# Kernel tuning notes

Measured on AMD Instinct MI355X. Metric: run time of the kernel, lower is better.

The kernel has to match this reference:

```python
import jax, jax.numpy as jnp
import numpy as np

C = 64        # number of classes (rows of mu)
K = 64        # int(d * overlap_ratio) = int(128 * 0.5)
ALPHA = 1.0   # margin


def _pairdist(mu, x):
    # Euclidean distance from every center to every sample: [C, N]
    d2 = (mu * mu).sum(-1)[:, None] + (x * x).sum(-1)[None, :] - 2.0 * (mu @ x.T)
    return jnp.sqrt(jnp.maximum(d2, 0.0))


def setup_inputs() -> dict:
    key = jax.random.key(0)
    k1, k2, k3 = jax.random.split(key, 3)
    N, D = 131072, 256
    x = jax.random.normal(k1, (N, D), dtype=jnp.float32)
    y = jax.random.randint(k2, (N, 3), 0, C)
    # ensure every class 0..C-1 is present with ~equal counts (matches torch.unique)
    y = y.at[:, 2].set(jnp.arange(N) % C)
    mu = jax.random.normal(k3, (C, D), dtype=jnp.float32)
    return {"x": x, "y": y, "mu": mu}


def reference(x, y, mu):
    labels = y[:, 2]                                     # [N]
    D = _pairdist(mu, x)                                 # [C, N]
    mask = labels[None, :] == jnp.arange(C)[:, None]     # [C, N] class membership

    # pos: per class c, K LARGEST distances from center c to its own samples
    pos_vals = jax.lax.top_k(jnp.where(mask, D, -jnp.inf), K)[0]  # [C, K]
    pos_mean = pos_vals.mean(-1)                                  # [C]

    # neg: for each sample-class c2, K SMALLEST distances from every center c1
    def neg_for_class(m):  # m: [N] bool mask for class c2
        vals = jax.lax.top_k(jnp.where(m[None, :], -D, -jnp.inf), K)[0]  # [C, K]
        return (-vals).mean(-1)  # [C] smallest-K mean per center c1

    negM = jax.lax.map(neg_for_class, mask)              # [C2, C1]

    hinge = jnp.maximum(ALPHA + pos_mean[None, :] - negM, 0.0)  # [C2, C1]
    offdiag = 1.0 - jnp.eye(C, dtype=hinge.dtype)
    loss = (hinge * offdiag).sum() / x.shape[0]
    return loss
```

## Files before the change

kernel.cpp:

```cpp
#include <hip/hip_runtime.h>
#include <math.h>


#define DDIM 256
#define CC 64
#define KSEL 64
#define TPTS 128
#define XS 40
#define SELN 2048

typedef short s4v __attribute__((ext_vector_type(4)));
typedef short s8v __attribute__((ext_vector_type(8)));
typedef float f4v __attribute__((ext_vector_type(4)));

__device__ __forceinline__ void cvt_split(float f, short& h, short& l) {
  const unsigned int u = __float_as_uint(f);
  const unsigned int hb = (u + 0x7FFFu + ((u >> 16) & 1u)) >> 16;
  h = (short)hb;
  const float rem = f - __uint_as_float(hb << 16);
  const unsigned int ur = __float_as_uint(rem);
  l = (short)((ur + 0x7FFFu + ((ur >> 16) & 1u)) >> 16);
}

__global__ __launch_bounds__(256) void prepK(const float* __restrict__ mu, short* __restrict__ mhG,
                                             short* __restrict__ mlG, float* __restrict__ mn2G,
                                             int* __restrict__ cnts) {
  const int b = blockIdx.x, t = threadIdx.x;
  if (b == 0 && t < 128) cnts[t] = 0;
  const int row = b * 4 + (t >> 6), l = t & 63;
  const float4 v = *reinterpret_cast<const float4*>(mu + (size_t)row * DDIM + l * 4);
  const float vs[4] = {v.x, v.y, v.z, v.w};
  s4v hv, lv;
  float s2 = 0.f;
  #pragma unroll
  for (int j = 0; j < 4; ++j) {
    short hj, lj; cvt_split(vs[j], hj, lj);
    hv[j] = hj; lv[j] = lj;
    s2 = fmaf(vs[j], vs[j], s2);
  }
  *reinterpret_cast<s4v*>(&mhG[(size_t)row * DDIM + l * 4]) = hv;
  *reinterpret_cast<s4v*>(&mlG[(size_t)row * DDIM + l * 4]) = lv;
  #pragma unroll
  for (int off = 32; off > 0; off >>= 1) s2 += __shfl_xor(s2, off, 64);
  if (l == 0) mn2G[row] = s2;
}

__global__ __launch_bounds__(256) void countK(const int* __restrict__ y, int* cnt, int N) {
  int i = blockIdx.x * 256 + threadIdx.x;
  if (i < N) atomicAdd(&cnt[y[3 * i + 2] & (CC - 1)], 1);
}

__global__ void scanK(const int* __restrict__ cnt, int* base) {
  if (threadIdx.x == 0) {
    int s = 0;
    for (int i = 0; i < CC; ++i) { base[i] = s; s += cnt[i]; }
  }
}

__global__ __launch_bounds__(256) void fillK(const int* __restrict__ y, const int* __restrict__ base,
                                             int* cnt2, int* idxs, int N) {
  int i = blockIdx.x * 256 + threadIdx.x;
  if (i < N) {
    int m = y[3 * i + 2] & (CC - 1);
    int r = atomicAdd(&cnt2[m], 1);
    idxs[base[m] + r] = i;
  }
}

__global__ __launch_bounds__(256, 4) void distK(const float* __restrict__ x, const short* __restrict__ mhG,
                                                const short* __restrict__ mlG, const float* __restrict__ mn2G,
                                                const int* __restrict__ idxs, float* __restrict__ Dg, int N) {
  __shared__ __align__(16) short xh[TPTS][XS];
  __shared__ __align__(16) short xl[TPTS][XS];
  __shared__ int pid[TPTS];
  __shared__ float xn2[TPTS];

  const int t = threadIdx.x;
  const int wgp0 = blockIdx.x * TPTS;
  if (t < TPTS) pid[t] = idxs[wgp0 + t];

  const int q = t & 7, pr = t >> 3;
  const int w = t >> 6, l = t & 63;
  const int lr = l & 15, lk = l >> 4;

  f4v acc[4][2];
  #pragma unroll
  for (int a = 0; a < 4; ++a)
    #pragma unroll
    for (int b = 0; b < 2; ++b) acc[a][b] = (f4v)0.f;
  float xnacc[4] = {0.f, 0.f, 0.f, 0.f};

  __syncthreads();
  int pidr[4];
  #pragma unroll
  for (int p = 0; p < 4; ++p) pidr[p] = pid[p * 32 + pr];

  float4 vreg[4];
  #pragma unroll
  for (int p = 0; p < 4; ++p)
    vreg[p] = *reinterpret_cast<const float4*>(x + (size_t)pidr[p] * DDIM + q * 4);

  for (int ch = 0; ch < 8; ++ch) {
    const int kb = ch * 32;
    s8v ah[4], al_[4];
    #pragma unroll
    for (int mt = 0; mt < 4; ++mt) {
      const size_t ro = (size_t)(mt * 16 + lr) * DDIM + kb + lk * 8;
      ah[mt]  = *reinterpret_cast<const s8v*>(mhG + ro);
      al_[mt] = *reinterpret_cast<const s8v*>(mlG + ro);
    }
    #pragma unroll
    for (int p = 0; p < 4; ++p) {
      const float vs[4] = {vreg[p].x, vreg[p].y, vreg[p].z, vreg[p].w};
      s4v hv, lv;
      float s2 = 0.f;
      #pragma unroll
      for (int j = 0; j < 4; ++j) {
        short hj, lj; cvt_split(vs[j], hj, lj);
        hv[j] = hj; lv[j] = lj;
        s2 = fmaf(vs[j], vs[j], s2);
      }
      xnacc[p] += s2;
      const int pt = p * 32 + pr;
      *reinterpret_cast<s4v*>(&xh[pt][q * 4]) = hv;
      *reinterpret_cast<s4v*>(&xl[pt][q * 4]) = lv;
    }
    __syncthreads();
    if (ch < 7) {
      #pragma unroll
      for (int p = 0; p < 4; ++p)
        vreg[p] = *reinterpret_cast<const float4*>(x + (size_t)pidr[p] * DDIM + kb + 32 + q * 4);
    }
    s8v bh[2], bl[2];
    #pragma unroll
    for (int nt = 0; nt < 2; ++nt) {
      const int prow = w * 32 + nt * 16 + lr;
      bh[nt] = *reinterpret_cast<const s8v*>(&xh[prow][lk * 8]);
      bl[nt] = *reinterpret_cast<const s8v*>(&xl[prow][lk * 8]);
    }
    #pragma unroll
    for (int mt = 0; mt < 4; ++mt) {
      #pragma unroll
      for (int nt = 0; nt < 2; ++nt) {
        acc[mt][nt] = __builtin_amdgcn_mfma_f32_16x16x32_bf16(ah[mt],  bh[nt], acc[mt][nt], 0, 0, 0);
        acc[mt][nt] = __builtin_amdgcn_mfma_f32_16x16x32_bf16(ah[mt],  bl[nt], acc[mt][nt], 0, 0, 0);
        acc[mt][nt] = __builtin_amdgcn_mfma_f32_16x16x32_bf16(al_[mt], bh[nt], acc[mt][nt], 0, 0, 0);
      }
    }
    __syncthreads();
  }
  #pragma unroll
  for (int p = 0; p < 4; ++p) {
    float s = xnacc[p];
    s += __shfl_xor(s, 1, 64); s += __shfl_xor(s, 2, 64); s += __shfl_xor(s, 4, 64);
    if (q == 0) xn2[p * 32 + pr] = s;
  }
  __syncthreads();
  #pragma unroll
  for (int mt = 0; mt < 4; ++mt) {
    #pragma unroll
    for (int r = 0; r < 4; ++r) {
      const int m = mt * 16 + lk * 4 + r;
      const float mn = mn2G[m];
      #pragma unroll
      for (int nt = 0; nt < 2; ++nt) {
        const int p = w * 32 + nt * 16 + lr;
        const float d2 = mn + xn2[p] - 2.f * acc[mt][nt][r];
        Dg[(size_t)m * N + wgp0 + p] = sqrtf(fmaxf(d2, 0.f));
      }
    }
  }
}

__global__ __launch_bounds__(128) void selK(const float* __restrict__ Dg, const int* __restrict__ cnt,
                                            const int* __restrict__ base, float* __restrict__ posM,
                                            float* __restrict__ neg, int N) {
  __shared__ __align__(16) unsigned int keys[SELN];
  __shared__ unsigned int sh_lo, sh_hi;
  __shared__ int sh_cnt[2];
  __shared__ float sh_sum[2];
  const int c = blockIdx.x, m = blockIdx.y;
  const int t = threadIdx.x;
  const int w = t >> 6, lane = t & 63;
  const bool diag = (c == m);
  int cm = cnt[m]; if (cm > SELN) cm = SELN;
  const int bm = base[m];
  const float* src = Dg + (size_t)c * N + bm;
  const int cm4 = (cm + 3) & ~3;

  unsigned int kmin = 0xFFFFFFFFu, kmax = 0u;
  for (int i = t; i < cm4; i += 128) {
    unsigned int key = 0xFFFFFFFFu;
    if (i < cm) {
      const unsigned int b = __float_as_uint(src[i]);
      key = diag ? ~b : b;
      kmin = min(kmin, key); kmax = max(kmax, key);
    }
    keys[i] = key;
  }
  #pragma unroll
  for (int off = 32; off > 0; off >>= 1) {
    kmin = min(kmin, (unsigned int)__shfl_xor((int)kmin, off, 64));
    kmax = max(kmax, (unsigned int)__shfl_xor((int)kmax, off, 64));
  }
  if (lane == 0) { sh_cnt[w] = (int)kmin; sh_sum[w] = __uint_as_float(kmax); }
  __syncthreads();
  if (t == 0) {
    sh_lo = min((unsigned int)sh_cnt[0], (unsigned int)sh_cnt[1]);
    sh_hi = max(__float_as_uint(sh_sum[0]), __float_as_uint(sh_sum[1]));
  }

  for (;;) {
    __syncthreads();
    const unsigned int lo = sh_lo, hi = sh_hi;
    if (lo >= hi) break;
    const unsigned int mid = lo + ((hi - lo) >> 1);
    int cl = 0;
    for (int i4 = t * 4; i4 < cm4; i4 += 512) {
      const uint4 kv = *reinterpret_cast<const uint4*>(&keys[i4]);
      cl += (int)(kv.x <= mid) + (int)(kv.y <= mid) + (int)(kv.z <= mid) + (int)(kv.w <= mid);
    }
    #pragma unroll
    for (int off = 32; off > 0; off >>= 1) cl += __shfl_xor(cl, off, 64);
    if (lane == 0) sh_cnt[w] = cl;
    __syncthreads();
    if (t == 0) {
      if (sh_cnt[0] + sh_cnt[1] >= KSEL) sh_hi = mid; else sh_lo = mid + 1;
    }
  }
  const unsigned int kth = sh_lo;

  int cl = 0; float sl = 0.f;
  for (int i4 = t * 4; i4 < cm4; i4 += 512) {
    const uint4 kv = *reinterpret_cast<const uint4*>(&keys[i4]);
    const unsigned int ks[4] = {kv.x, kv.y, kv.z, kv.w};
    #pragma unroll
    for (int j = 0; j < 4; ++j) {
      if (ks[j] < kth) { ++cl; sl += __uint_as_float(diag ? ~ks[j] : ks[j]); }
    }
  }
  #pragma unroll
  for (int off = 32; off > 0; off >>= 1) {
    cl += __shfl_xor(cl, off, 64);
    sl += __shfl_xor(sl, off, 64);
  }
  if (lane == 0) { sh_cnt[w] = cl; sh_sum[w] = sl; }
  __syncthreads();
  if (t == 0) {
    const int totc = sh_cnt[0] + sh_cnt[1];
    const float tots = sh_sum[0] + sh_sum[1];
    const float kval = __uint_as_float(diag ? ~kth : kth);
    const float mval = (tots + (float)(KSEL - totc) * kval) * (1.0f / KSEL);
    if (diag) posM[c] = mval; else neg[m * CC + c] = mval;
  }
}

__global__ __launch_bounds__(256) void lossK(const float* __restrict__ posM, const float* __restrict__ neg,
                                             float* __restrict__ out, int N) {
  __shared__ float red[256];
  const int t = threadIdx.x;
  float s = 0.f;
  for (int idx = t; idx < CC * CC; idx += 256) {
    const int m = idx >> 6, c = idx & 63;
    if (m != c) {
      const float h = 1.0f + posM[c] - neg[idx];
      s += fmaxf(h, 0.0f);
    }
  }
  red[t] = s;
  __syncthreads();
  for (int off = 128; off > 0; off >>= 1) {
    if (t < off) red[t] += red[t + off];
    __syncthreads();
  }
  if (t == 0) out[0] = red[0] / (float)N;
}

__global__ void wsFailK(float* out) {
  if (threadIdx.x == 0) out[0] = -1.0e30f;
}

extern "C" void kernel_launch(void* const* d_in, const int* in_sizes, int n_in,
                              void* d_out, int out_size, void* d_ws, size_t ws_size,
                              hipStream_t stream) {
  const float* x  = (const float*)d_in[0];
  const int*   y  = (const int*)d_in[1];
  const float* mu = (const float*)d_in[2];
  float* out = (float*)d_out;
  const int N = in_sizes[0] / DDIM;

  const size_t need = (size_t)655360 + (size_t)CC * (size_t)N * 4;
  if (ws_size < need) {
    hipLaunchKernelGGL(wsFailK, dim3(1), dim3(64), 0, stream, out);
    return;
  }
  char* w = (char*)d_ws;
  int*   cnt  = (int*)(w);
  int*   cnt2 = (int*)(w + 256);
  int*   base = (int*)(w + 512);
  float* posM = (float*)(w + 768);
  float* neg  = (float*)(w + 1024);
  float* mn2G = (float*)(w + 17408);
  short* mhG  = (short*)(w + 20480);
  short* mlG  = (short*)(w + 53248);
  int*   idxs = (int*)(w + 131072);
  float* Dg   = (float*)(w + 655360);

  hipLaunchKernelGGL(prepK, dim3(16), dim3(256), 0, stream, mu, mhG, mlG, mn2G, cnt);
  hipLaunchKernelGGL(countK, dim3((N + 255) / 256), dim3(256), 0, stream, y, cnt, N);
  hipLaunchKernelGGL(scanK, dim3(1), dim3(64), 0, stream, cnt, base);
  hipLaunchKernelGGL(fillK, dim3((N + 255) / 256), dim3(256), 0, stream, y, base, cnt2, idxs, N);
  hipLaunchKernelGGL(distK, dim3(N / TPTS), dim3(256), 0, stream, x, mhG, mlG, mn2G, idxs, Dg, N);
  hipLaunchKernelGGL(selK, dim3(CC, CC), dim3(128), 0, stream, Dg, cnt, base, posM, neg, N);
  hipLaunchKernelGGL(lossK, dim3(1), dim3(256), 0, stream, posM, neg, out, N);
}
```

Before: 331.3 us.

## Stage full x rows in LDS once and shrink distance tile to 64 points

The distance kernel now loads each gathered x row whole (all 256 dims), splits it into bf16 hi/lo and stores it in a padded LDS tile in one pass. This replaces the chunked load/convert/sync loop with a single barrier before the MFMA loop. The tile shrinks from 128 to 64 points, so each wave owns 16 points, and occupancy hints drop to 2 blocks per CU because LDS use grows. This aims to remove the per-chunk barriers and their serialization, at the cost of larger LDS per block, more blocks, and no overlap of global loads with MFMA work.

```diff
diff --git a/kernel.cpp b/kernel.cpp
--- a/kernel.cpp
+++ b/kernel.cpp
@@ -5,8 +5,8 @@
 #define DDIM 256
 #define CC 64
 #define KSEL 64
-#define TPTS 128
-#define XS 40
+#define TPTS 64
+#define XS3 264
 #define SELN 2048
 
 typedef short s4v __attribute__((ext_vector_type(4)));
@@ -67,11 +67,11 @@
   }
 }
 
-__global__ __launch_bounds__(256, 4) void distK(const float* __restrict__ x, const short* __restrict__ mhG,
+__global__ __launch_bounds__(256, 2) void distK(const float* __restrict__ x, const short* __restrict__ mhG,
                                                 const short* __restrict__ mlG, const float* __restrict__ mn2G,
                                                 const int* __restrict__ idxs, float* __restrict__ Dg, int N) {
-  __shared__ __align__(16) short xh[TPTS][XS];
-  __shared__ __align__(16) short xl[TPTS][XS];
+  __shared__ __align__(16) short xh[TPTS][XS3];
+  __shared__ __align__(16) short xl[TPTS][XS3];
   __shared__ int pid[TPTS];
   __shared__ float xn2[TPTS];
 
@@ -79,27 +79,43 @@
   const int wgp0 = blockIdx.x * TPTS;
   if (t < TPTS) pid[t] = idxs[wgp0 + t];
 
-  const int q = t & 7, pr = t >> 3;
   const int w = t >> 6, l = t & 63;
   const int lr = l & 15, lk = l >> 4;
-
-  f4v acc[4][2];
-  #pragma unroll
-  for (int a = 0; a < 4; ++a)
-    #pragma unroll
-    for (int b = 0; b < 2; ++b) acc[a][b] = (f4v)0.f;
-  float xnacc[4] = {0.f, 0.f, 0.f, 0.f};
-
-  __syncthreads();
-  int pidr[4];
-  #pragma unroll
-  for (int p = 0; p < 4; ++p) pidr[p] = pid[p * 32 + pr];
-
-  float4 vreg[4];
-  #pragma unroll
-  for (int p = 0; p < 4; ++p)
-    vreg[p] = *reinterpret_cast<const float4*>(x + (size_t)pidr[p] * DDIM + q * 4);
-
+  const int c8 = t & 7;
+
+  __syncthreads();
+
+  #pragma unroll
+  for (int pass = 0; pass < 2; ++pass) {
+    const int row = pass * 32 + (t >> 3);
+    const size_t rbase = (size_t)pid[row] * DDIM;
+    float s2 = 0.f;
+    #pragma unroll
+    for (int j = 0; j < 8; ++j) {
+      const int fi = (c8 + 8 * j) * 4;
+      const float4 v = *reinterpret_cast<const float4*>(x + rbase + fi);
+      const float vs[4] = {v.x, v.y, v.z, v.w};
+      s4v hv, lv;
+      #pragma unroll
+      for (int jj = 0; jj < 4; ++jj) {
+        short hj, lj; cvt_split(vs[jj], hj, lj);
+        hv[jj] = hj; lv[jj] = lj;
+        s2 = fmaf(vs[jj], vs[jj], s2);
+      }
+      *reinterpret_cast<s4v*>(&xh[row][fi]) = hv;
+      *reinterpret_cast<s4v*>(&xl[row][fi]) = lv;
+    }
+    s2 += __shfl_xor(s2, 1, 64); s2 += __shfl_xor(s2, 2, 64); s2 += __shfl_xor(s2, 4, 64);
+    if (c8 == 0) xn2[row] = s2;
+  }
+  __syncthreads();
+
+  f4v acc[4];
+  #pragma unroll
+  for (int a = 0; a < 4; ++a) acc[a] = (f4v)0.f;
+  const int prow = w * 16 + lr;
+
+  #pragma unroll
   for (int ch = 0; ch < 8; ++ch) {
     const int kb = ch * 32;
     s8v ah[4], al_[4];
@@ -109,65 +125,27 @@
       ah[mt]  = *reinterpret_cast<const s8v*>(mhG + ro);
       al_[mt] = *reinterpret_cast<const s8v*>(mlG + ro);
     }
-    #pragma unroll
-    for (int p = 0; p < 4; ++p) {
-      const float vs[4] = {vreg[p].x, vreg[p].y, vreg[p].z, vreg[p].w};
-      s4v hv, lv;
-      float s2 = 0.f;
-      #pragma unroll
-      for (int j = 0; j < 4; ++j) {
-        short hj, lj; cvt_split(vs[j], hj, lj);
-        hv[j] = hj; lv[j] = lj;
-        s2 = fmaf(vs[j], vs[j], s2);
-      }
-      xnacc[p] += s2;
-      const int pt = p * 32 + pr;
-      *reinterpret_cast<s4v*>(&xh[pt][q * 4]) = hv;
-      *reinterpret_cast<s4v*>(&xl[pt][q * 4]) = lv;
-    }
-    __syncthreads();
-    if (ch < 7) {
-      #pragma unroll
-      for (int p = 0; p < 4; ++p)
-        vreg[p] = *reinterpret_cast<const float4*>(x + (size_t)pidr[p] * DDIM + kb + 32 + q * 4);
-    }
-    s8v bh[2], bl[2];
-    #pragma unroll
-    for (int nt = 0; nt < 2; ++nt) {
-      const int prow = w * 32 + nt * 16 + lr;
-      bh[nt] = *reinterpret_cast<const s8v*>(&xh[prow][lk * 8]);
-      bl[nt] = *reinterpret_cast<const s8v*>(&xl[prow][lk * 8]);
-    }
-    #pragma unroll
-    for (int mt = 0; mt < 4; ++mt) {
-      #pragma unroll
-      for (int nt = 0; nt < 2; ++nt) {
-        acc[mt][nt] = __builtin_amdgcn_mfma_f32_16x16x32_bf16(ah[mt],  bh[nt], acc[mt][nt], 0, 0, 0);
-        acc[mt][nt] = __builtin_amdgcn_mfma_f32_16x16x32_bf16(ah[mt],  bl[nt], acc[mt][nt], 0, 0, 0);
-        acc[mt][nt] = __builtin_amdgcn_mfma_f32_16x16x32_bf16(al_[mt], bh[nt], acc[mt][nt], 0, 0, 0);
-      }
-    }
-    __syncthreads();
-  }
-  #pragma unroll
-  for (int p = 0; p < 4; ++p) {
-    float s = xnacc[p];
-    s += __shfl_xor(s, 1, 64); s += __shfl_xor(s, 2, 64); s += __shfl_xor(s, 4, 64);
-    if (q == 0) xn2[p * 32 + pr] = s;
-  }
-  __syncthreads();
+    const s8v bh = *reinterpret_cast<const s8v*>(&xh[prow][kb + lk * 8]);
+    const s8v bl = *reinterpret_cast<const s8v*>(&xl[prow][kb + lk * 8]);
+    #pragma unroll
+    for (int mt = 0; mt < 4; ++mt)
+      acc[mt] = __builtin_amdgcn_mfma_f32_16x16x32_bf16(ah[mt], bh, acc[mt], 0, 0, 0);
+    #pragma unroll
+    for (int mt = 0; mt < 4; ++mt)
+      acc[mt] = __builtin_amdgcn_mfma_f32_16x16x32_bf16(ah[mt], bl, acc[mt], 0, 0, 0);
+    #pragma unroll
+    for (int mt = 0; mt < 4; ++mt)
+      acc[mt] = __builtin_amdgcn_mfma_f32_16x16x32_bf16(al_[mt], bh, acc[mt], 0, 0, 0);
+  }
+
+  const float xn = xn2[prow];
   #pragma unroll
   for (int mt = 0; mt < 4; ++mt) {
     #pragma unroll
     for (int r = 0; r < 4; ++r) {
       const int m = mt * 16 + lk * 4 + r;
-      const float mn = mn2G[m];
-      #pragma unroll
-      for (int nt = 0; nt < 2; ++nt) {
-        const int p = w * 32 + nt * 16 + lr;
-        const float d2 = mn + xn2[p] - 2.f * acc[mt][nt][r];
-        Dg[(size_t)m * N + wgp0 + p] = sqrtf(fmaxf(d2, 0.f));
-      }
+      const float d2 = mn2G[m] + xn - 2.f * acc[mt][r];
+      Dg[(size_t)m * N + wgp0 + prow] = sqrtf(fmaxf(d2, 0.f));
     }
   }
 }
```

Measured after the change: 372.9 us. 12.5% more time.
